# Kernel tuning notes

Hardware: AMD Instinct MI355X
Metric: run time of the kernel (lower is better)

Reference implementation:

```python
import jax, jax.numpy as jnp
import numpy as np

B = 2048
D = 256
TEMPERATURE = 0.5
EPS = 1e-8  # torch.nn.CosineSimilarity eps


def _neg_indices(b):
    # Static mask: exclude diagonal and positive pairs (i, B+i), (B+i, i).
    n = 2 * b
    mask = np.ones((n, n), dtype=bool)
    np.fill_diagonal(mask, False)
    idx = np.arange(b)
    mask[idx, b + idx] = False
    mask[b + idx, idx] = False
    rows, cols = np.nonzero(mask)  # row-major order, matches torch sim[mask]
    return rows.reshape(n, n - 2), cols.reshape(n, n - 2)

_NEG_ROWS, _NEG_COLS = _neg_indices(B)


def setup_inputs() -> dict:
    key = jax.random.key(0)
    k1, k2 = jax.random.split(key)
    z_i = jax.random.normal(k1, (B, D), dtype=jnp.float32)
    z_j = jax.random.normal(k2, (B, D), dtype=jnp.float32)
    return {"z_i": z_i, "z_j": z_j}


def reference(z_i, z_j):
    b = z_i.shape[0]
    n = 2 * b
    z = jnp.concatenate([z_i, z_j], axis=0)  # [N, D]
    # Cosine similarity = normalize -> matmul (same math as broadcast CosineSimilarity)
    norm = jnp.maximum(jnp.linalg.norm(z, axis=1, keepdims=True), EPS)
    zn = z / norm
    sim = (zn @ zn.T) / TEMPERATURE  # [N, N]
    # positives: diag(sim, B) and diag(sim, -B)
    pos = jnp.concatenate([jnp.diagonal(sim, offset=b), jnp.diagonal(sim, offset=-b)], axis=0)  # [N]
    # negatives: static masked gather -> [N, N-2]
    neg = sim[_NEG_ROWS, _NEG_COLS]
    logits = jnp.concatenate([pos[:, None], neg], axis=1)  # [N, N-1]
    # CrossEntropyLoss(reduction='sum') with labels all zero, then / N
    loss = -jax.nn.log_softmax(logits, axis=1)[:, 0]
    return jnp.sum(loss) / n
```

## Files before the change

### kernel.cpp

```cpp
#include <hip/hip_runtime.h>
#include <hip/hip_bf16.h>
#include <math.h>

#define B_PAIRS 2048
#define N_ROWS  4096
#define D_DIM   256
#define INV_T   2.0f

typedef __attribute__((ext_vector_type(4))) float  floatx4;


__device__ __forceinline__ void async_copy16(const void* gsrc, void* ldst) {
    __builtin_amdgcn_global_load_lds(
        (__attribute__((address_space(1))) void*)gsrc,
        (__attribute__((address_space(3))) void*)ldst,
        16, 0, 0);
}

__global__ __launch_bounds__(256)
void ntx_normalize(const float* __restrict__ z_i,
                   const float* __restrict__ z_j,
                   unsigned* __restrict__ zn8,
                   float* __restrict__ S,
                   float* __restrict__ posSum) {
    const int w    = threadIdx.x >> 6;
    const int lane = threadIdx.x & 63;
    const int row  = blockIdx.x * 4 + w;
    const float* src = (row < B_PAIRS) ? (z_i + (size_t)row * D_DIM)
                                       : (z_j + (size_t)(row - B_PAIRS) * D_DIM);
    const float4 v = *(const float4*)(src + lane * 4);
    float ss = v.x * v.x + v.y * v.y + v.z * v.z + v.w * v.w;
    #pragma unroll
    for (int off = 32; off > 0; off >>= 1) ss += __shfl_xor(ss, off, 64);
    const float rn = 1.0f / fmaxf(sqrtf(ss), 1e-8f);
    unsigned pk = 0;
    pk = __builtin_amdgcn_cvt_pk_fp8_f32(v.x * rn, v.y * rn, pk, false);
    pk = __builtin_amdgcn_cvt_pk_fp8_f32(v.z * rn, v.w * rn, pk, true);
    zn8[(size_t)row * (D_DIM / 4) + lane] = pk;
    if (lane == 0) S[row] = 0.0f;
    if (blockIdx.x == 0 && threadIdx.x == 0) *posSum = 0.0f;
}

#define BM 128
#define BN 128
#define BK 32
#define N_TILES 528

__global__ __launch_bounds__(256)
void ntx_simtile(const unsigned char* __restrict__ zn8,
                 float* __restrict__ S,
                 float* __restrict__ posSum) {
    __shared__ __align__(16) unsigned char As[BM * BK];
    __shared__ __align__(16) unsigned char Bs[BN * BK];

    int t = blockIdx.x, by = 0, rowlen = 32;
    while (t >= rowlen) { t -= rowlen; by++; rowlen--; }
    const int bx = by + t;

    const int tid  = threadIdx.x;
    const int lane = tid & 63;
    const int w    = tid >> 6;
    const int wr   = w >> 1;
    const int wc   = w & 1;
    const int quad = lane >> 4;
    const int l16  = lane & 15;

    const int rowA0 = by * BM;
    const int rowB0 = bx * BN;
    const bool isDiag = (rowA0 == rowB0);
    const bool isPos  = (rowB0 == (rowA0 ^ B_PAIRS));

    floatx4 acc[4][4];
    #pragma unroll
    for (int i = 0; i < 4; i++)
        #pragma unroll
        for (int j = 0; j < 4; j++)
            acc[i][j] = (floatx4){0.f, 0.f, 0.f, 0.f};

    for (int k0 = 0; k0 < D_DIM; k0 += BK) {
        const int r  = tid >> 1;
        const int kc = tid & 1;
        async_copy16(zn8 + ((size_t)(rowA0 + r) * D_DIM + k0 + kc * 16),
                     As + tid * 16);
        async_copy16(zn8 + ((size_t)(rowB0 + r) * D_DIM + k0 + kc * 16),
                     Bs + tid * 16);
        __syncthreads();

        long afr[4], bfr[4];
        #pragma unroll
        for (int fi = 0; fi < 4; fi++) {
            const int ar = wr * 64 + fi * 16 + l16;
            afr[fi] = *(const long*)(const void*)(As + ar * BK + quad * 8);
        }
        #pragma unroll
        for (int fj = 0; fj < 4; fj++) {
            const int br = wc * 64 + fj * 16 + l16;
            bfr[fj] = *(const long*)(const void*)(Bs + br * BK + quad * 8);
        }
        #pragma unroll
        for (int fi = 0; fi < 4; fi++)
            #pragma unroll
            for (int fj = 0; fj < 4; fj++)
                acc[fi][fj] = __builtin_amdgcn_mfma_f32_16x16x32_fp8_fp8(
                    afr[fi], bfr[fj], acc[fi][fj], 0, 0, 0);
        __syncthreads();
    }

    float cs[4] = {0.f, 0.f, 0.f, 0.f};
    float psum = 0.f;
    #pragma unroll
    for (int fi = 0; fi < 4; fi++) {
        float rs[4] = {0.f, 0.f, 0.f, 0.f};
        #pragma unroll
        for (int fj = 0; fj < 4; fj++) {
            const int rj = wc * 64 + fj * 16 + l16;
            #pragma unroll
            for (int reg = 0; reg < 4; reg++) {
                const int ri = wr * 64 + fi * 16 + quad * 4 + reg;
                const float v = acc[fi][fj][reg] * INV_T;
                const bool d = (ri == rj);
                if (isPos && d) psum += 2.0f * v;
                const float e = (isDiag && d) ? 0.f : __expf(v);
                rs[reg] += e;
                cs[fj]  += e;
            }
        }
        #pragma unroll
        for (int reg = 0; reg < 4; reg++) {
            float r = rs[reg];
            r += __shfl_xor(r, 1, 16);
            r += __shfl_xor(r, 2, 16);
            r += __shfl_xor(r, 4, 16);
            r += __shfl_xor(r, 8, 16);
            if (l16 == 0)
                atomicAdd(&S[rowA0 + wr * 64 + fi * 16 + quad * 4 + reg], r);
        }
    }
    if (!isDiag) {
        #pragma unroll
        for (int fj = 0; fj < 4; fj++) {
            float c = cs[fj];
            c += __shfl_xor(c, 16, 64);
            c += __shfl_xor(c, 32, 64);
            if (quad == 0)
                atomicAdd(&S[rowB0 + wc * 64 + fj * 16 + l16], c);
        }
    }
    if (isPos) {
        psum += __shfl_xor(psum, 1, 64);  psum += __shfl_xor(psum, 2, 64);
        psum += __shfl_xor(psum, 4, 64);  psum += __shfl_xor(psum, 8, 64);
        psum += __shfl_xor(psum, 16, 64); psum += __shfl_xor(psum, 32, 64);
        __shared__ float pred[4];
        if (lane == 0) pred[w] = psum;
        __syncthreads();
        if (tid == 0)
            atomicAdd(posSum, pred[0] + pred[1] + pred[2] + pred[3]);
    }
}

__global__ __launch_bounds__(1024)
void ntx_finalize(const float* __restrict__ S,
                  const float* __restrict__ posSum,
                  float* __restrict__ out) {
    const int tid = threadIdx.x;
    float acc = 0.f;
    #pragma unroll
    for (int c = 0; c < 4; c++)
        acc += __logf(S[tid + c * 1024]);
    #pragma unroll
    for (int off = 32; off > 0; off >>= 1) acc += __shfl_xor(acc, off, 64);
    __shared__ float red[16];
    if ((tid & 63) == 0) red[tid >> 6] = acc;
    __syncthreads();
    if (tid == 0) {
        float s = 0.f;
        #pragma unroll
        for (int k = 0; k < 16; k++) s += red[k];
        out[0] = (s - *posSum) / (float)N_ROWS;
    }
}

extern "C" void kernel_launch(void* const* d_in, const int* in_sizes, int n_in,
                              void* d_out, int out_size, void* d_ws, size_t ws_size,
                              hipStream_t stream) {
    const float* z_i = (const float*)d_in[0];
    const float* z_j = (const float*)d_in[1];
    float* out = (float*)d_out;

    unsigned char* zn8 = (unsigned char*)d_ws;
    float* S      = (float*)((char*)d_ws + (size_t)N_ROWS * D_DIM);
    float* posSum = S + N_ROWS;

    ntx_normalize<<<N_ROWS / 4, 256, 0, stream>>>(z_i, z_j, (unsigned*)zn8, S, posSum);
    ntx_simtile<<<N_TILES, 256, 0, stream>>>(zn8, S, posSum);
    ntx_finalize<<<1, 1024, 0, stream>>>(S, posSum, out);
}
```

Baseline: 80.72 us.

## Load MFMA fragments directly from global memory, dropping LDS staging and barriers

Removes the shared-memory tiles and async global-to-LDS copies in the similarity-tile kernel. Each wave now loads its fp8 A/B fragments straight from global memory (through L2/L1) in a fully unrolled K loop with no __syncthreads. This removes barrier stalls and LDS round trips and lets the compiler hoist loads early. The cost is redundant global loads across waves, since each row fragment is fetched by two waves, and 8-byte strided accesses that rely on the cache.

```diff
diff --git a/kernel.cpp b/kernel.cpp
--- a/kernel.cpp
+++ b/kernel.cpp
@@ -9,13 +9,6 @@
 
 typedef __attribute__((ext_vector_type(4))) float  floatx4;
 
-
-__device__ __forceinline__ void async_copy16(const void* gsrc, void* ldst) {
-    __builtin_amdgcn_global_load_lds(
-        (__attribute__((address_space(1))) void*)gsrc,
-        (__attribute__((address_space(3))) void*)ldst,
-        16, 0, 0);
-}
 
 __global__ __launch_bounds__(256)
 void ntx_normalize(const float* __restrict__ z_i,
@@ -43,16 +36,12 @@
 
 #define BM 128
 #define BN 128
-#define BK 32
 #define N_TILES 528
 
 __global__ __launch_bounds__(256)
 void ntx_simtile(const unsigned char* __restrict__ zn8,
                  float* __restrict__ S,
                  float* __restrict__ posSum) {
-    __shared__ __align__(16) unsigned char As[BM * BK];
-    __shared__ __align__(16) unsigned char Bs[BN * BK];
-
     int t = blockIdx.x, by = 0, rowlen = 32;
     while (t >= rowlen) { t -= rowlen; by++; rowlen--; }
     const int bx = by + t;
@@ -70,6 +59,14 @@
     const bool isDiag = (rowA0 == rowB0);
     const bool isPos  = (rowB0 == (rowA0 ^ B_PAIRS));
 
+    const unsigned char* aP[4];
+    const unsigned char* bP[4];
+    #pragma unroll
+    for (int f = 0; f < 4; f++) {
+        aP[f] = zn8 + (size_t)(rowA0 + wr * 64 + f * 16 + l16) * D_DIM + quad * 8;
+        bP[f] = zn8 + (size_t)(rowB0 + wc * 64 + f * 16 + l16) * D_DIM + quad * 8;
+    }
+
     floatx4 acc[4][4];
     #pragma unroll
     for (int i = 0; i < 4; i++)
@@ -77,25 +74,13 @@
         for (int j = 0; j < 4; j++)
             acc[i][j] = (floatx4){0.f, 0.f, 0.f, 0.f};
 
-    for (int k0 = 0; k0 < D_DIM; k0 += BK) {
-        const int r  = tid >> 1;
-        const int kc = tid & 1;
-        async_copy16(zn8 + ((size_t)(rowA0 + r) * D_DIM + k0 + kc * 16),
-                     As + tid * 16);
-        async_copy16(zn8 + ((size_t)(rowB0 + r) * D_DIM + k0 + kc * 16),
-                     Bs + tid * 16);
-        __syncthreads();
-
+    #pragma unroll
+    for (int step = 0; step < D_DIM / 32; step++) {
         long afr[4], bfr[4];
         #pragma unroll
-        for (int fi = 0; fi < 4; fi++) {
-            const int ar = wr * 64 + fi * 16 + l16;
-            afr[fi] = *(const long*)(const void*)(As + ar * BK + quad * 8);
-        }
-        #pragma unroll
-        for (int fj = 0; fj < 4; fj++) {
-            const int br = wc * 64 + fj * 16 + l16;
-            bfr[fj] = *(const long*)(const void*)(Bs + br * BK + quad * 8);
+        for (int f = 0; f < 4; f++) {
+            afr[f] = *(const long*)(const void*)(aP[f] + step * 32);
+            bfr[f] = *(const long*)(const void*)(bP[f] + step * 32);
         }
         #pragma unroll
         for (int fi = 0; fi < 4; fi++)
@@ -103,7 +88,6 @@
             for (int fj = 0; fj < 4; fj++)
                 acc[fi][fj] = __builtin_amdgcn_mfma_f32_16x16x32_fp8_fp8(
                     afr[fi], bfr[fj], acc[fi][fj], 0, 0, 0);
-        __syncthreads();
     }
 
     float cs[4] = {0.f, 0.f, 0.f, 0.f};
```

Result: slower. 90.91 us (+12.6%).

## Store fp8 embeddings k-slab-major and load full K into LDS at once

Applied to the files above, without the earlier changes.

The normalize kernel now writes the fp8 embeddings in a layout of eight 32-byte k-slabs, each holding all rows contiguously. The similarity tile kernel then issues all eight async copies per operand up front, waits on a single barrier, and runs the full K loop from LDS with no per-step barriers. Each load is now contiguous per slab, and the sixteen barriers of the old K loop are gone. In exchange, LDS use grows to 64 KB per block, which may cut occupancy, and the MFMA work can no longer overlap with loading.

```diff
diff --git a/kernel.cpp b/kernel.cpp
--- a/kernel.cpp
+++ b/kernel.cpp
@@ -20,7 +20,7 @@
 __global__ __launch_bounds__(256)
 void ntx_normalize(const float* __restrict__ z_i,
                    const float* __restrict__ z_j,
-                   unsigned* __restrict__ zn8,
+                   unsigned* __restrict__ zn8t,
                    float* __restrict__ S,
                    float* __restrict__ posSum) {
     const int w    = threadIdx.x >> 6;
@@ -36,22 +36,21 @@
     unsigned pk = 0;
     pk = __builtin_amdgcn_cvt_pk_fp8_f32(v.x * rn, v.y * rn, pk, false);
     pk = __builtin_amdgcn_cvt_pk_fp8_f32(v.z * rn, v.w * rn, pk, true);
-    zn8[(size_t)row * (D_DIM / 4) + lane] = pk;
+    zn8t[(size_t)(lane >> 3) * 32768 + row * 8 + (lane & 7)] = pk;
     if (lane == 0) S[row] = 0.0f;
     if (blockIdx.x == 0 && threadIdx.x == 0) *posSum = 0.0f;
 }
 
 #define BM 128
 #define BN 128
-#define BK 32
 #define N_TILES 528
 
 __global__ __launch_bounds__(256)
-void ntx_simtile(const unsigned char* __restrict__ zn8,
+void ntx_simtile(const unsigned char* __restrict__ zn8t,
                  float* __restrict__ S,
                  float* __restrict__ posSum) {
-    __shared__ __align__(16) unsigned char As[BM * BK];
-    __shared__ __align__(16) unsigned char Bs[BN * BK];
+    __shared__ __align__(16) unsigned char As[8 * 128 * 32];
+    __shared__ __align__(16) unsigned char Bs[8 * 128 * 32];
 
     int t = blockIdx.x, by = 0, rowlen = 32;
     while (t >= rowlen) { t -= rowlen; by++; rowlen--; }
@@ -67,8 +66,17 @@
 
     const int rowA0 = by * BM;
     const int rowB0 = bx * BN;
-    const bool isDiag = (rowA0 == rowB0);
+    const bool isDiag = (by == bx);
     const bool isPos  = (rowB0 == (rowA0 ^ B_PAIRS));
+
+    #pragma unroll
+    for (int s = 0; s < 8; s++) {
+        async_copy16(zn8t + (size_t)s * 131072 + rowA0 * 32 + tid * 16,
+                     As + s * 4096 + tid * 16);
+        async_copy16(zn8t + (size_t)s * 131072 + rowB0 * 32 + tid * 16,
+                     Bs + s * 4096 + tid * 16);
+    }
+    __syncthreads();
 
     floatx4 acc[4][4];
     #pragma unroll
@@ -77,25 +85,18 @@
         for (int j = 0; j < 4; j++)
             acc[i][j] = (floatx4){0.f, 0.f, 0.f, 0.f};
 
-    for (int k0 = 0; k0 < D_DIM; k0 += BK) {
-        const int r  = tid >> 1;
-        const int kc = tid & 1;
-        async_copy16(zn8 + ((size_t)(rowA0 + r) * D_DIM + k0 + kc * 16),
-                     As + tid * 16);
-        async_copy16(zn8 + ((size_t)(rowB0 + r) * D_DIM + k0 + kc * 16),
-                     Bs + tid * 16);
-        __syncthreads();
-
+    #pragma unroll
+    for (int s = 0; s < 8; s++) {
         long afr[4], bfr[4];
         #pragma unroll
         for (int fi = 0; fi < 4; fi++) {
             const int ar = wr * 64 + fi * 16 + l16;
-            afr[fi] = *(const long*)(const void*)(As + ar * BK + quad * 8);
+            afr[fi] = *(const long*)(const void*)(As + s * 4096 + ar * 32 + quad * 8);
         }
         #pragma unroll
         for (int fj = 0; fj < 4; fj++) {
             const int br = wc * 64 + fj * 16 + l16;
-            bfr[fj] = *(const long*)(const void*)(Bs + br * BK + quad * 8);
+            bfr[fj] = *(const long*)(const void*)(Bs + s * 4096 + br * 32 + quad * 8);
         }
         #pragma unroll
         for (int fi = 0; fi < 4; fi++)
@@ -103,7 +104,6 @@
             for (int fj = 0; fj < 4; fj++)
                 acc[fi][fj] = __builtin_amdgcn_mfma_f32_16x16x32_fp8_fp8(
                     afr[fi], bfr[fj], acc[fi][fj], 0, 0, 0);
-        __syncthreads();
     }
 
     float cs[4] = {0.f, 0.f, 0.f, 0.f};
@@ -187,11 +187,11 @@
     const float* z_j = (const float*)d_in[1];
     float* out = (float*)d_out;
 
-    unsigned char* zn8 = (unsigned char*)d_ws;
+    unsigned char* zn8t = (unsigned char*)d_ws;
     float* S      = (float*)((char*)d_ws + (size_t)N_ROWS * D_DIM);
     float* posSum = S + N_ROWS;
 
-    ntx_normalize<<<N_ROWS / 4, 256, 0, stream>>>(z_i, z_j, (unsigned*)zn8, S, posSum);
-    ntx_simtile<<<N_TILES, 256, 0, stream>>>(zn8, S, posSum);
+    ntx_normalize<<<N_ROWS / 4, 256, 0, stream>>>(z_i, z_j, (unsigned*)zn8t, S, posSum);
+    ntx_simtile<<<N_TILES, 256, 0, stream>>>(zn8t, S, posSum);
     ntx_finalize<<<1, 1024, 0, stream>>>(S, posSum, out);
 }
```

Result: faster. 76.76 us (median of 2 runs) (-4.9%).
